# Optimization experiments

Hardware: AMD Instinct MI355X
Metric: run time of the kernel (lower is better)

The kernel has to match this reference:

```python
import jax, jax.numpy as jnp
import numpy as np

B, S, D = 16, 2048, 64
SCALE = 1.0 / np.sqrt(np.float32(D))  # forward divides by sqrt(embedding_dim=64)


def setup_inputs() -> dict:
    key = jax.random.key(0)
    ks = jax.random.split(key, 7)
    return {
        "x": jax.random.normal(ks[0], (B, S, D), dtype=jnp.float32),
        "Wq": jax.random.normal(ks[1], (D, D), dtype=jnp.float32) * 0.02,
        "bq": jax.random.normal(ks[2], (D,), dtype=jnp.float32) * 0.02,
        "Wk": jax.random.normal(ks[3], (D, D), dtype=jnp.float32) * 0.02,
        "bk": jax.random.normal(ks[4], (D,), dtype=jnp.float32) * 0.02,
        "Wv": jax.random.normal(ks[5], (D, D), dtype=jnp.float32) * 0.02,
        "bv": jax.random.normal(ks[6], (D,), dtype=jnp.float32) * 0.02,
    }


def reference(x, Wq, bq, Wk, bk, Wv, bv):
    # Linear projections (weights stored [in, out], math-equivalent to nn.Linear)
    q = jnp.einsum("bsd,de->bse", x, Wq) + bq
    k = jnp.einsum("bsd,de->bse", x, Wk) + bk
    v = jnp.einsum("bsd,de->bse", x, Wv) + bv
    # Unfused scores: [B, S, S]
    scores = jnp.einsum("bqd,bkd->bqk", q, k) * jnp.float32(SCALE)
    causal = jnp.tril(jnp.ones((S, S), dtype=bool))  # mask[:S,:S]
    scores = jnp.where(causal, scores, jnp.float32(-jnp.inf))
    attn = jax.nn.softmax(scores, axis=-1)
    # dropout is identity in eval mode (reference baseline)
    out = jnp.einsum("bqk,bkd->bqd", attn, v)
    return out
```

## Files before the change

### kernel.cpp

```cpp
#include <hip/hip_runtime.h>

#define NB 16
#define SS 2048
#define DD 64

typedef __attribute__((ext_vector_type(8))) short short8;
typedef __attribute__((ext_vector_type(4))) float f32x4;

#define SCL2E 0.18033688011112042f

__device__ __forceinline__ short f2bf(float f) {
  union { float f; unsigned u; } v; v.f = f;
  unsigned r = (v.u + 0x7fffu + ((v.u >> 16) & 1u)) >> 16;
  return (short)r;
}

__device__ __forceinline__ unsigned cvtpk_bf16(float lo, float hi) {
  unsigned r;
  asm("v_cvt_pk_bf16_f32 %0, %1, %2" : "=v"(r) : "v"(lo), "v"(hi));
  return r;
}

__device__ __forceinline__ short8 load_a_frag_f32(const float* p) {
  float4 u = *(const float4*)p;
  float4 w = *(const float4*)(p + 4);
  short8 r;
  r[0] = f2bf(u.x); r[1] = f2bf(u.y); r[2] = f2bf(u.z); r[3] = f2bf(u.w);
  r[4] = f2bf(w.x); r[5] = f2bf(w.y); r[6] = f2bf(w.z); r[7] = f2bf(w.w);
  return r;
}

__global__ __launch_bounds__(256) void wprep_kernel(
    const float* __restrict__ Wq, const float* __restrict__ Wk,
    const float* __restrict__ Wv, ushort* __restrict__ Wt)
{
  const float* Ws[3] = {Wq, Wk, Wv};
  const int m = blockIdx.x;
  const float* src = Ws[m];
  ushort* dst = Wt + m * 4096;
  const int t = threadIdx.x;
#pragma unroll
  for (int i = 0; i < 4; ++i) {
    int idx = i * 1024 + t * 4;
    int k = idx >> 6, n0 = idx & 63;
    float4 w4 = *(const float4*)(src + idx);
    dst[(n0 + 0) * 64 + k] = (ushort)f2bf(w4.x);
    dst[(n0 + 1) * 64 + k] = (ushort)f2bf(w4.y);
    dst[(n0 + 2) * 64 + k] = (ushort)f2bf(w4.z);
    dst[(n0 + 3) * 64 + k] = (ushort)f2bf(w4.w);
  }
}

__global__ __launch_bounds__(256) void proj_kernel(
    const float* __restrict__ x, const ushort* __restrict__ Wt,
    const float* __restrict__ bq, const float* __restrict__ bk,
    const float* __restrict__ bv,
    ushort* __restrict__ qo, ushort* __restrict__ ko, ushort* __restrict__ vT)
{
  __shared__ __align__(16) ushort Vs[64][68];
  const int t = threadIdx.x;
  const int lane = t & 63, w = t >> 6;
  const int l15 = lane & 15, quad = lane >> 4;
  const int g = blockIdx.x * 64 + w * 16 + l15;
  short8 b0 = load_a_frag_f32(x + (size_t)g * 64 + quad * 8);
  short8 b1 = load_a_frag_f32(x + (size_t)g * 64 + 32 + quad * 8);
  const int lrow = w * 16 + l15;

#pragma unroll
  for (int m = 0; m < 3; ++m) {
    const float* bp = (m == 0 ? bq : (m == 1 ? bk : bv));
    const ushort* wm = Wt + m * 4096;
#pragma unroll
    for (int nt = 0; nt < 4; ++nt) {
      const ushort* ap = wm + (nt * 16 + l15) * 64 + quad * 8;
      short8 a0 = *(const short8*)ap;
      short8 a1 = *(const short8*)(ap + 32);
      f32x4 acc = {0.f, 0.f, 0.f, 0.f};
      acc = __builtin_amdgcn_mfma_f32_16x16x32_bf16(a0, b0, acc, 0, 0, 0);
      acc = __builtin_amdgcn_mfma_f32_16x16x32_bf16(a1, b1, acc, 0, 0, 0);
      float4 bb = *(const float4*)(bp + nt * 16 + quad * 4);
      unsigned p0 = cvtpk_bf16(acc[0] + bb.x, acc[1] + bb.y);
      unsigned p1 = cvtpk_bf16(acc[2] + bb.z, acc[3] + bb.w);
      uint2 pk; pk.x = p0; pk.y = p1;
      if (m == 0) {
        *(uint2*)(qo + (size_t)g * 64 + nt * 16 + quad * 4) = pk;
      } else if (m == 1) {
        *(uint2*)(ko + (size_t)g * 64 + nt * 16 + quad * 4) = pk;
      } else {
        *(uint2*)&Vs[lrow][nt * 16 + quad * 4] = pk;
      }
    }
  }
  __syncthreads();
  {
    const int batch = blockIdx.x >> 5;
    const int s0 = (blockIdx.x & 31) * 64;
    const int d = t >> 2, j0 = (t & 3) * 16;
    ushort tmp[16];
#pragma unroll
    for (int j = 0; j < 16; ++j) tmp[j] = Vs[j0 + j][d];
    ushort* dst = vT + (size_t)batch * DD * SS + (size_t)d * SS + s0 + j0;
    ((int4*)dst)[0] = ((int4*)tmp)[0];
    ((int4*)dst)[1] = ((int4*)tmp)[1];
  }
}

__device__ __forceinline__ short8 build_pa(unsigned A0, unsigned A1,
                                           unsigned B0, unsigned B1, int quad) {
  int xA0 = __shfl_xor((int)A0, 32);
  int xA1 = __shfl_xor((int)A1, 32);
  int xB0 = __shfl_xor((int)B0, 32);
  int xB1 = __shfl_xor((int)B1, 32);
  const bool hi = quad >= 2;
  const bool odd = quad & 1;
  int Lo0 = hi ? xB0 : (int)A0;
  int Lo1 = hi ? xB1 : (int)A1;
  int Hi0 = hi ? (int)B0 : xA0;
  int Hi1 = hi ? (int)B1 : xA1;
  int xLo0 = __shfl_xor(Lo0, 16);
  int xLo1 = __shfl_xor(Lo1, 16);
  int xHi0 = __shfl_xor(Hi0, 16);
  int xHi1 = __shfl_xor(Hi1, 16);
  int4 wv;
  wv.x = odd ? xHi0 : Lo0;
  wv.y = odd ? xHi1 : Lo1;
  wv.z = odd ? Hi0 : xLo0;
  wv.w = odd ? Hi1 : xLo1;
  return *(short8*)&wv;
}

template<bool MASKED>
__device__ __forceinline__ void attn_half(
    const f32x4 (&c)[4], float& l_acc, f32x4 (&acc)[4],
    const short8 (&vf0)[4], const short8 (&vf1)[4],
    int keybase, int qabs, int quad)
{
  unsigned pk[4][2];
#pragma unroll
  for (int ct = 0; ct < 4; ++ct) {
    float pe[4];
#pragma unroll
    for (int r = 0; r < 4; ++r) {
      float p = __builtin_amdgcn_exp2f(c[ct][r] * SCL2E);
      if (MASKED && (keybase + ct * 16 + quad * 4 + r > qabs)) p = 0.f;
      pe[r] = p;
      l_acc += p;
    }
    pk[ct][0] = cvtpk_bf16(pe[0], pe[1]);
    pk[ct][1] = cvtpk_bf16(pe[2], pe[3]);
  }
  short8 pa0 = build_pa(pk[0][0], pk[0][1], pk[1][0], pk[1][1], quad);
  short8 pa1 = build_pa(pk[2][0], pk[2][1], pk[3][0], pk[3][1], quad);
  __builtin_amdgcn_s_setprio(1);
#pragma unroll
  for (int nt = 0; nt < 4; ++nt) {
    acc[nt] = __builtin_amdgcn_mfma_f32_16x16x32_bf16(pa0, vf0[nt], acc[nt], 0, 0, 0);
    acc[nt] = __builtin_amdgcn_mfma_f32_16x16x32_bf16(pa1, vf1[nt], acc[nt], 0, 0, 0);
  }
  __builtin_amdgcn_s_setprio(0);
}

__global__ __launch_bounds__(256, 3) void attn_kernel(
    const ushort* __restrict__ qg, const ushort* __restrict__ kg,
    const ushort* __restrict__ vT, float* __restrict__ out)
{
  __shared__ __align__(16) float accW[4][32][68];
  __shared__ float lW[4][32];

  const int t = threadIdx.x, bid = blockIdx.x;
  const int batch = (bid & 7) * 2 + ((bid >> 3) & 1);
  const int qt = 63 - (bid >> 4);
  const int q0 = qt * 32;
  const int lane = t & 63, w = t >> 6;
  const int l15 = lane & 15, quad = lane >> 4;
  const size_t bbase = (size_t)batch * SS * DD;

  const ushort* qp = qg + bbase + (size_t)(q0 + l15) * 64 + quad * 8;
  short8 a0 = *(const short8*)qp;
  short8 a1 = *(const short8*)(qp + 32);
  short8 a2 = *(const short8*)(qp + 16 * 64);
  short8 a3 = *(const short8*)(qp + 16 * 64 + 32);

  f32x4 acc0[4], acc1[4];
  float l0 = 0.f, l1 = 0.f;
#pragma unroll
  for (int nt = 0; nt < 4; ++nt) {
    acc0[nt] = (f32x4){0.f, 0.f, 0.f, 0.f};
    acc1[nt] = (f32x4){0.f, 0.f, 0.f, 0.f};
  }

  const int ktotal = ((q0 + 31) >> 6) + 1;
  const ushort* kp0 = kg + bbase + (size_t)(w * 64 + l15) * 64 + quad * 8;
  const ushort* kp1 = kp0 + 2048;
  const ushort* vp0 = vT + bbase + (size_t)(l15) * SS + w * 64 + quad * 8;
  const ushort* vp1 = vp0 + 16 * SS;
  const ushort* vp2 = vp0 + 32 * SS;
  const ushort* vp3 = vp0 + 48 * SS;

  const int qabs0 = q0 + l15, qabs1 = q0 + 16 + l15;

  for (int kt = w; kt < ktotal; kt += 4) {
    short8 kf0[4], kf1[4], vf0[4], vf1[4];
    kf0[0] = *(const short8*)(kp0);
    kf1[0] = *(const short8*)(kp0 + 32);
    kf0[1] = *(const short8*)(kp0 + 1024);
    kf1[1] = *(const short8*)(kp0 + 1056);
    kf0[2] = *(const short8*)(kp1);
    kf1[2] = *(const short8*)(kp1 + 32);
    kf0[3] = *(const short8*)(kp1 + 1024);
    kf1[3] = *(const short8*)(kp1 + 1056);
    vf0[0] = *(const short8*)(vp0); vf1[0] = *(const short8*)(vp0 + 32);
    vf0[1] = *(const short8*)(vp1); vf1[1] = *(const short8*)(vp1 + 32);
    vf0[2] = *(const short8*)(vp2); vf1[2] = *(const short8*)(vp2 + 32);
    vf0[3] = *(const short8*)(vp3); vf1[3] = *(const short8*)(vp3 + 32);

    f32x4 c0[4], c1[4];
    __builtin_amdgcn_s_setprio(1);
#pragma unroll
    for (int ct = 0; ct < 4; ++ct) {
      f32x4 z = {0.f, 0.f, 0.f, 0.f};
      c0[ct] = __builtin_amdgcn_mfma_f32_16x16x32_bf16(kf0[ct], a0, z, 0, 0, 0);
      c0[ct] = __builtin_amdgcn_mfma_f32_16x16x32_bf16(kf1[ct], a1, c0[ct], 0, 0, 0);
      c1[ct] = __builtin_amdgcn_mfma_f32_16x16x32_bf16(kf0[ct], a2, z, 0, 0, 0);
      c1[ct] = __builtin_amdgcn_mfma_f32_16x16x32_bf16(kf1[ct], a3, c1[ct], 0, 0, 0);
    }
    __builtin_amdgcn_s_setprio(0);

    const int kb = kt * 64;
    if (kt == ktotal - 1) {
      attn_half<true >(c0, l0, acc0, vf0, vf1, kb, qabs0, quad);
      attn_half<true >(c1, l1, acc1, vf0, vf1, kb, qabs1, quad);
    } else {
      attn_half<false>(c0, l0, acc0, vf0, vf1, kb, qabs0, quad);
      attn_half<false>(c1, l1, acc1, vf0, vf1, kb, qabs1, quad);
    }
    kp0 += 16384; kp1 += 16384;
    vp0 += 256; vp1 += 256; vp2 += 256; vp3 += 256;
  }

  l0 += __shfl_xor(l0, 16); l0 += __shfl_xor(l0, 32);
  l1 += __shfl_xor(l1, 16); l1 += __shfl_xor(l1, 32);

#pragma unroll
  for (int r = 0; r < 4; ++r)
#pragma unroll
    for (int nt = 0; nt < 4; ++nt) {
      accW[w][quad * 4 + r][nt * 16 + l15] = acc0[nt][r];
      accW[w][16 + quad * 4 + r][nt * 16 + l15] = acc1[nt][r];
    }
  if (lane < 16) {
    lW[w][lane] = l0;
    lW[w][16 + lane] = l1;
  }
  __syncthreads();

  {
    const int row = t >> 3, col0 = (t & 7) * 8;
    float den = lW[0][row] + lW[1][row] + lW[2][row] + lW[3][row];
    float iv = 1.0f / den;
    float4 oa = {0.f, 0.f, 0.f, 0.f}, ob = {0.f, 0.f, 0.f, 0.f};
#pragma unroll
    for (int ww = 0; ww < 4; ++ww) {
      float4 x0 = *(const float4*)&accW[ww][row][col0];
      float4 x1 = *(const float4*)&accW[ww][row][col0 + 4];
      oa.x += x0.x; oa.y += x0.y; oa.z += x0.z; oa.w += x0.w;
      ob.x += x1.x; ob.y += x1.y; ob.z += x1.z; ob.w += x1.w;
    }
    oa.x *= iv; oa.y *= iv; oa.z *= iv; oa.w *= iv;
    ob.x *= iv; ob.y *= iv; ob.z *= iv; ob.w *= iv;
    float* op = out + bbase + (size_t)(q0 + row) * 64 + col0;
    *(float4*)op = oa;
    *(float4*)(op + 4) = ob;
  }
}

extern "C" void kernel_launch(void* const* d_in, const int* in_sizes, int n_in,
                              void* d_out, int out_size, void* d_ws, size_t ws_size,
                              hipStream_t stream) {
  (void)in_sizes; (void)n_in; (void)out_size; (void)ws_size;
  const float* x  = (const float*)d_in[0];
  const float* Wq = (const float*)d_in[1];
  const float* bq = (const float*)d_in[2];
  const float* Wk = (const float*)d_in[3];
  const float* bk = (const float*)d_in[4];
  const float* Wv = (const float*)d_in[5];
  const float* bv = (const float*)d_in[6];
  float* out = (float*)d_out;

  ushort* qws = (ushort*)d_ws;
  ushort* kws = qws + (size_t)NB * SS * DD;
  ushort* vws = kws + (size_t)NB * SS * DD;
  ushort* wt  = vws + (size_t)NB * SS * DD;

  wprep_kernel<<<dim3(3), dim3(256), 0, stream>>>(Wq, Wk, Wv, wt);
  proj_kernel<<<dim3(NB * SS / 64), dim3(256), 0, stream>>>(
      x, wt, bq, bk, bv, qws, kws, vws);
  attn_kernel<<<dim3(NB * (SS / 32)), dim3(256), 0, stream>>>(
      qws, kws, vws, out);
}
```

Measured before the change: 122.7 us.

## Fuse weight prep into projection, halve attention LDS reduction buffer, raise occupancy

Result: slower. 126.3 us (+2.9%).

```diff
diff --git a/kernel.cpp b/kernel.cpp
--- a/kernel.cpp
+++ b/kernel.cpp
@@ -30,64 +30,57 @@
   return r;
 }
 
-__global__ __launch_bounds__(256) void wprep_kernel(
-    const float* __restrict__ Wq, const float* __restrict__ Wk,
-    const float* __restrict__ Wv, ushort* __restrict__ Wt)
-{
-  const float* Ws[3] = {Wq, Wk, Wv};
-  const int m = blockIdx.x;
-  const float* src = Ws[m];
-  ushort* dst = Wt + m * 4096;
-  const int t = threadIdx.x;
-#pragma unroll
-  for (int i = 0; i < 4; ++i) {
-    int idx = i * 1024 + t * 4;
-    int k = idx >> 6, n0 = idx & 63;
-    float4 w4 = *(const float4*)(src + idx);
-    dst[(n0 + 0) * 64 + k] = (ushort)f2bf(w4.x);
-    dst[(n0 + 1) * 64 + k] = (ushort)f2bf(w4.y);
-    dst[(n0 + 2) * 64 + k] = (ushort)f2bf(w4.z);
-    dst[(n0 + 3) * 64 + k] = (ushort)f2bf(w4.w);
-  }
-}
-
 __global__ __launch_bounds__(256) void proj_kernel(
-    const float* __restrict__ x, const ushort* __restrict__ Wt,
-    const float* __restrict__ bq, const float* __restrict__ bk,
-    const float* __restrict__ bv,
+    const float* __restrict__ x,
+    const float* __restrict__ Wq, const float* __restrict__ bq,
+    const float* __restrict__ Wk, const float* __restrict__ bk,
+    const float* __restrict__ Wv, const float* __restrict__ bv,
     ushort* __restrict__ qo, ushort* __restrict__ ko, ushort* __restrict__ vT)
 {
+  __shared__ __align__(16) ushort Wt[3][64][72];
   __shared__ __align__(16) ushort Vs[64][68];
   const int t = threadIdx.x;
+  {
+    const float* Ws[3] = {Wq, Wk, Wv};
+    for (int m = 0; m < 3; ++m)
+      for (int i = 0; i < 4; ++i) {
+        int idx = i * 1024 + t * 4;
+        int kk = idx >> 6, n0 = idx & 63;
+        float4 w4 = *(const float4*)(Ws[m] + kk * 64 + n0);
+        Wt[m][n0 + 0][kk] = (ushort)f2bf(w4.x);
+        Wt[m][n0 + 1][kk] = (ushort)f2bf(w4.y);
+        Wt[m][n0 + 2][kk] = (ushort)f2bf(w4.z);
+        Wt[m][n0 + 3][kk] = (ushort)f2bf(w4.w);
+      }
+  }
+  __syncthreads();
+
   const int lane = t & 63, w = t >> 6;
   const int l15 = lane & 15, quad = lane >> 4;
   const int g = blockIdx.x * 64 + w * 16 + l15;
-  short8 b0 = load_a_frag_f32(x + (size_t)g * 64 + quad * 8);
-  short8 b1 = load_a_frag_f32(x + (size_t)g * 64 + 32 + quad * 8);
-  const int lrow = w * 16 + l15;
-
-#pragma unroll
+  short8 a0 = load_a_frag_f32(x + (size_t)g * 64 + quad * 8);
+  short8 a1 = load_a_frag_f32(x + (size_t)g * 64 + 32 + quad * 8);
+  const int lrow0 = w * 16 + quad * 4;
+  const int row0 = blockIdx.x * 64 + lrow0;
+
   for (int m = 0; m < 3; ++m) {
     const float* bp = (m == 0 ? bq : (m == 1 ? bk : bv));
-    const ushort* wm = Wt + m * 4096;
-#pragma unroll
     for (int nt = 0; nt < 4; ++nt) {
-      const ushort* ap = wm + (nt * 16 + l15) * 64 + quad * 8;
-      short8 a0 = *(const short8*)ap;
-      short8 a1 = *(const short8*)(ap + 32);
+      short8 b0 = *(const short8*)&Wt[m][nt * 16 + l15][quad * 8];
+      short8 b1 = *(const short8*)&Wt[m][nt * 16 + l15][32 + quad * 8];
       f32x4 acc = {0.f, 0.f, 0.f, 0.f};
       acc = __builtin_amdgcn_mfma_f32_16x16x32_bf16(a0, b0, acc, 0, 0, 0);
       acc = __builtin_amdgcn_mfma_f32_16x16x32_bf16(a1, b1, acc, 0, 0, 0);
-      float4 bb = *(const float4*)(bp + nt * 16 + quad * 4);
-      unsigned p0 = cvtpk_bf16(acc[0] + bb.x, acc[1] + bb.y);
-      unsigned p1 = cvtpk_bf16(acc[2] + bb.z, acc[3] + bb.w);
-      uint2 pk; pk.x = p0; pk.y = p1;
+      float bb = bp[nt * 16 + l15];
       if (m == 0) {
-        *(uint2*)(qo + (size_t)g * 64 + nt * 16 + quad * 4) = pk;
+        for (int r = 0; r < 4; ++r)
+          qo[(size_t)(row0 + r) * 64 + nt * 16 + l15] = (ushort)f2bf(acc[r] + bb);
       } else if (m == 1) {
-        *(uint2*)(ko + (size_t)g * 64 + nt * 16 + quad * 4) = pk;
+        for (int r = 0; r < 4; ++r)
+          ko[(size_t)(row0 + r) * 64 + nt * 16 + l15] = (ushort)f2bf(acc[r] + bb);
       } else {
-        *(uint2*)&Vs[lrow][nt * 16 + quad * 4] = pk;
+        for (int r = 0; r < 4; ++r)
+          Vs[lrow0 + r][nt * 16 + l15] = (ushort)f2bf(acc[r] + bb);
       }
     }
   }
@@ -97,7 +90,6 @@
     const int s0 = (blockIdx.x & 31) * 64;
     const int d = t >> 2, j0 = (t & 3) * 16;
     ushort tmp[16];
-#pragma unroll
     for (int j = 0; j < 16; ++j) tmp[j] = Vs[j0 + j][d];
     ushort* dst = vT + (size_t)batch * DD * SS + (size_t)d * SS + s0 + j0;
     ((int4*)dst)[0] = ((int4*)tmp)[0];
@@ -160,11 +152,11 @@
   __builtin_amdgcn_s_setprio(0);
 }
 
-__global__ __launch_bounds__(256, 3) void attn_kernel(
+__global__ __launch_bounds__(256, 4) void attn_kernel(
     const ushort* __restrict__ qg, const ushort* __restrict__ kg,
     const ushort* __restrict__ vT, float* __restrict__ out)
 {
-  __shared__ __align__(16) float accW[4][32][68];
+  __shared__ __align__(16) float accW[2][32][68];
   __shared__ float lW[4][32];
 
   const int t = threadIdx.x, bid = blockIdx.x;
@@ -241,16 +233,28 @@
   l0 += __shfl_xor(l0, 16); l0 += __shfl_xor(l0, 32);
   l1 += __shfl_xor(l1, 16); l1 += __shfl_xor(l1, 32);
 
-#pragma unroll
-  for (int r = 0; r < 4; ++r)
-#pragma unroll
-    for (int nt = 0; nt < 4; ++nt) {
-      accW[w][quad * 4 + r][nt * 16 + l15] = acc0[nt][r];
-      accW[w][16 + quad * 4 + r][nt * 16 + l15] = acc1[nt][r];
-    }
   if (lane < 16) {
     lW[w][lane] = l0;
     lW[w][16 + lane] = l1;
+  }
+  if (w < 2) {
+#pragma unroll
+    for (int r = 0; r < 4; ++r)
+#pragma unroll
+      for (int nt = 0; nt < 4; ++nt) {
+        accW[w][quad * 4 + r][nt * 16 + l15] = acc0[nt][r];
+        accW[w][16 + quad * 4 + r][nt * 16 + l15] = acc1[nt][r];
+      }
+  }
+  __syncthreads();
+  if (w >= 2) {
+#pragma unroll
+    for (int r = 0; r < 4; ++r)
+#pragma unroll
+      for (int nt = 0; nt < 4; ++nt) {
+        accW[w - 2][quad * 4 + r][nt * 16 + l15] += acc0[nt][r];
+        accW[w - 2][16 + quad * 4 + r][nt * 16 + l15] += acc1[nt][r];
+      }
   }
   __syncthreads();
 
@@ -258,13 +262,14 @@
     const int row = t >> 3, col0 = (t & 7) * 8;
     float den = lW[0][row] + lW[1][row] + lW[2][row] + lW[3][row];
     float iv = 1.0f / den;
-    float4 oa = {0.f, 0.f, 0.f, 0.f}, ob = {0.f, 0.f, 0.f, 0.f};
-#pragma unroll
-    for (int ww = 0; ww < 4; ++ww) {
-      float4 x0 = *(const float4*)&accW[ww][row][col0];
-      float4 x1 = *(const float4*)&accW[ww][row][col0 + 4];
-      oa.x += x0.x; oa.y += x0.y; oa.z += x0.z; oa.w += x0.w;
-      ob.x += x1.x; ob.y += x1.y; ob.z += x1.z; ob.w += x1.w;
+    float4 oa, ob;
+    {
+      float4 x0 = *(const float4*)&accW[0][row][col0];
+      float4 x1 = *(const float4*)&accW[0][row][col0 + 4];
+      float4 y0 = *(const float4*)&accW[1][row][col0];
+      float4 y1 = *(const float4*)&accW[1][row][col0 + 4];
+      oa.x = x0.x + y0.x; oa.y = x0.y + y0.y; oa.z = x0.z + y0.z; oa.w = x0.w + y0.w;
+      ob.x = x1.x + y1.x; ob.y = x1.y + y1.y; ob.z = x1.z + y1.z; ob.w = x1.w + y1.w;
     }
     oa.x *= iv; oa.y *= iv; oa.z *= iv; oa.w *= iv;
     ob.x *= iv; ob.y *= iv; ob.z *= iv; ob.w *= iv;
@@ -290,11 +295,9 @@
   ushort* qws = (ushort*)d_ws;
   ushort* kws = qws + (size_t)NB * SS * DD;
   ushort* vws = kws + (size_t)NB * SS * DD;
-  ushort* wt  = vws + (size_t)NB * SS * DD;
-
-  wprep_kernel<<<dim3(3), dim3(256), 0, stream>>>(Wq, Wk, Wv, wt);
+
   proj_kernel<<<dim3(NB * SS / 64), dim3(256), 0, stream>>>(
-      x, wt, bq, bk, bv, qws, kws, vws);
+      x, Wq, bq, Wk, bk, Wv, bv, qws, kws, vws);
   attn_kernel<<<dim3(NB * (SS / 32)), dim3(256), 0, stream>>>(
       qws, kws, vws, out);
 }
```
